# Kernel tuning notes

Hardware: AMD Instinct MI355X
Metric: run time of the kernel (lower is better)

Reference implementation:

```python
import jax, jax.numpy as jnp
import numpy as np

N_NODES = 100000
N_EDGES = 3200000
D = 256
REPEAT = 2
FACTOR = 0.5


def setup_inputs() -> dict:
    key = jax.random.key(0)
    k1, k2, k3, k4, k5, k6 = jax.random.split(key, 6)
    x = jax.random.normal(k1, (N_NODES, D), dtype=jnp.float32)
    vals = jax.random.uniform(k2, (N_EDGES,), dtype=jnp.float32)
    # Xavier-ish scale for linear weights
    W0 = jax.random.normal(k3, (D, D), dtype=jnp.float32) / np.sqrt(D)
    W1 = jax.random.normal(k4, (D, D), dtype=jnp.float32) / np.sqrt(D)
    rows = jax.random.randint(k5, (N_EDGES,), 0, N_NODES, dtype=jnp.int32)
    cols = jax.random.randint(k6, (N_EDGES,), 0, N_NODES, dtype=jnp.int32)
    return {"x": x, "vals": vals, "W0": W0, "W1": W1, "rows": rows, "cols": cols}


def reference(x, vals, W0, W1, rows, cols):
    # support is sparse [N, N] in COO: support[rows[e], cols[e]] = vals[e]
    def spmm(h):
        # gather source-node features, scale by edge weight, scatter-add to dst
        return jax.ops.segment_sum(vals[:, None] * h[cols], rows,
                                   num_segments=N_NODES)

    h = x
    for W, act in ((W0, jax.nn.relu), (W1, lambda v: v)):
        # _propagate: repeated SpMM with scalar factor
        for _ in range(REPEAT):
            h = spmm(h) * FACTOR
        # linear (no bias) + activation
        h = act(h @ W)
    return h
```

## Files before the change

kernel.cpp:

```cpp
#include <hip/hip_runtime.h>
#include <hip/hip_bf16.h>
#include <hip/hip_fp16.h>

#define N_D 256
#define NBLK 832
#define CPB 52
#define NCH 16
#define RPG_MAX 12512

typedef __attribute__((ext_vector_type(8))) short bf16x8;
typedef __attribute__((ext_vector_type(4))) float f32x4;

__device__ __forceinline__ unsigned short f2bf(float f) {
  union { float f; unsigned u; } c; c.f = f;
  unsigned u = c.u;
  return (unsigned short)((u + 0x7fffu + ((u >> 16) & 1u)) >> 16);
}
__device__ __forceinline__ float asf(unsigned u) {
  union { unsigned u; float f; } c; c.u = u;
  return c.f;
}
__device__ __forceinline__ int grp_of(int r, unsigned gmagic) {
  int g = (int)(((unsigned long long)(unsigned)r * gmagic) >> 37);
  return min(g, 7);
}

template <bool AF32>
__device__ __forceinline__ void gemm_core(
    const void* __restrict__ H, const unsigned short* __restrict__ WT,
    unsigned short* __restrict__ C, int M, int bid) {
  const int wave = threadIdx.x >> 6;
  const int lane = threadIdx.x & 63;
  const int m = lane & 15;
  const int p = lane >> 4;
  const int row0 = bid * 128 + wave * 32;

  f32x4 acc0[16], acc1[16];
#pragma unroll
  for (int i = 0; i < 16; ++i) {
    acc0[i] = (f32x4){0.f, 0.f, 0.f, 0.f};
    acc1[i] = (f32x4){0.f, 0.f, 0.f, 0.f};
  }

  const int r0 = row0 + m;
  const int r1 = row0 + 16 + m;
  const bool ok0 = r0 < M, ok1 = r1 < M;

  for (int k0 = 0; k0 < N_D; k0 += 32) {
    bf16x8 a0 = {0,0,0,0,0,0,0,0}, a1 = {0,0,0,0,0,0,0,0};
    if (AF32) {
      if (ok0) {
        const float* ap = (const float*)H + (size_t)r0 * N_D + k0 + p * 8;
        const float4 f0 = *reinterpret_cast<const float4*>(ap);
        const float4 f1 = *reinterpret_cast<const float4*>(ap + 4);
        a0[0]=f2bf(f0.x); a0[1]=f2bf(f0.y); a0[2]=f2bf(f0.z); a0[3]=f2bf(f0.w);
        a0[4]=f2bf(f1.x); a0[5]=f2bf(f1.y); a0[6]=f2bf(f1.z); a0[7]=f2bf(f1.w);
      }
      if (ok1) {
        const float* ap = (const float*)H + (size_t)r1 * N_D + k0 + p * 8;
        const float4 f0 = *reinterpret_cast<const float4*>(ap);
        const float4 f1 = *reinterpret_cast<const float4*>(ap + 4);
        a1[0]=f2bf(f0.x); a1[1]=f2bf(f0.y); a1[2]=f2bf(f0.z); a1[3]=f2bf(f0.w);
        a1[4]=f2bf(f1.x); a1[5]=f2bf(f1.y); a1[6]=f2bf(f1.z); a1[7]=f2bf(f1.w);
      }
    } else {
      if (ok0) a0 = *reinterpret_cast<const bf16x8*>(
          (const unsigned short*)H + (size_t)r0 * N_D + k0 + p * 8);
      if (ok1) a1 = *reinterpret_cast<const bf16x8*>(
          (const unsigned short*)H + (size_t)r1 * N_D + k0 + p * 8);
    }
#pragma unroll
    for (int nt = 0; nt < 16; ++nt) {
      const bf16x8 b = *reinterpret_cast<const bf16x8*>(
          WT + (size_t)(nt * 16 + m) * N_D + k0 + p * 8);
      acc0[nt] = __builtin_amdgcn_mfma_f32_16x16x32_bf16(a0, b, acc0[nt], 0, 0, 0);
      acc1[nt] = __builtin_amdgcn_mfma_f32_16x16x32_bf16(a1, b, acc1[nt], 0, 0, 0);
    }
  }

#pragma unroll
  for (int nt = 0; nt < 16; ++nt) {
    const int col = nt * 16 + m;
#pragma unroll
    for (int rr = 0; rr < 4; ++rr) {
      const int ra = row0 + p * 4 + rr;
      const int rb = ra + 16;
      if (ra < M) C[(size_t)ra * N_D + col] = f2bf(acc0[nt][rr]);
      if (rb < M) C[(size_t)rb * N_D + col] = f2bf(acc1[nt][rr]);
    }
  }
}

__global__ __launch_bounds__(256) void gemm3_bf16(
    const unsigned short* __restrict__ H, const unsigned short* __restrict__ WT,
    unsigned short* __restrict__ C, int M) {
  gemm_core<false>(H, WT, C, M, blockIdx.x);
}

__global__ __launch_bounds__(256) void p0_kernel(
    const int* __restrict__ rows, int* __restrict__ cntT,
    int n_edges, unsigned gmagic,
    const float* __restrict__ W0, const float* __restrict__ W1,
    unsigned short* __restrict__ WT0, unsigned short* __restrict__ WT1) {
  if (blockIdx.x >= NBLK) {
    const int b = blockIdx.x - NBLK;
    const int w = b >> 8;
    const int k = b & 255;
    const int n = threadIdx.x;
    const float* W = w ? W1 : W0;
    unsigned short* WT = w ? WT1 : WT0;
    WT[(size_t)n * N_D + k] = f2bf(W[(size_t)k * N_D + n]);
    return;
  }
  __shared__ int l8[8];
  if (threadIdx.x < 8) l8[threadIdx.x] = 0;
  __syncthreads();
  for (int e = blockIdx.x * 256 + threadIdx.x; e < n_edges; e += NBLK * 256) {
    atomicAdd(&l8[grp_of(rows[e], gmagic)], 1);
  }
  __syncthreads();
  if (threadIdx.x < 8) cntT[threadIdx.x * NBLK + blockIdx.x] = l8[threadIdx.x];
}

__global__ __launch_bounds__(256) void scan_one(
    const int* __restrict__ in, int* __restrict__ out, int n) {
  __shared__ int swsum[4];
  __shared__ int carry_sh;
  const int tid = threadIdx.x;
  const int lane = tid & 63;
  const int wid = tid >> 6;
  if (tid == 0) carry_sh = 0;
  __syncthreads();
  for (int base = 0; base < n; base += 1024) {
    const int i0 = base + tid * 4;
    int4 v = make_int4(0, 0, 0, 0);
    if (i0 + 3 < n) v = *reinterpret_cast<const int4*>(in + i0);
    else {
      if (i0     < n) v.x = in[i0];
      if (i0 + 1 < n) v.y = in[i0 + 1];
      if (i0 + 2 < n) v.z = in[i0 + 2];
    }
    const int s1 = v.x, s2 = s1 + v.y, s3 = s2 + v.z, s4 = s3 + v.w;
    int ws = s4;
#pragma unroll
    for (int off = 1; off < 64; off <<= 1) {
      int o = __shfl_up(ws, off, 64);
      if (lane >= off) ws += o;
    }
    if (lane == 63) swsum[wid] = ws;
    __syncthreads();
    if (wid == 0) {
      int t = (lane < 4) ? swsum[lane] : 0;
#pragma unroll
      for (int off = 1; off < 4; off <<= 1) {
        int o = __shfl_up(t, off, 64);
        if (lane >= off) t += o;
      }
      if (lane < 4) swsum[lane] = t;
    }
    __syncthreads();
    const int carry = carry_sh;
    const int tbase = carry + (wid ? swsum[wid - 1] : 0) + ws - s4;
    if (i0     < n) out[i0]     = tbase;
    if (i0 + 1 < n) out[i0 + 1] = tbase + s1;
    if (i0 + 2 < n) out[i0 + 2] = tbase + s2;
    if (i0 + 3 < n) out[i0 + 3] = tbase + s3;
    __syncthreads();
    if (tid == 0) carry_sh = carry + swsum[3];
    __syncthreads();
  }
  if (tid == 0) out[n] = carry_sh;
}

__global__ __launch_bounds__(256) void fatpg_kernel(
    const int* __restrict__ rows, const int* __restrict__ cols,
    const float* __restrict__ vals, const int* __restrict__ pofsT,
    int2* __restrict__ part, int n_edges, unsigned gmagic,
    const float* __restrict__ x, const unsigned short* __restrict__ WT0,
    unsigned short* __restrict__ hB, int M) {
  if (blockIdx.x >= NBLK) {
    gemm_core<true>(x, WT0, hB, M, blockIdx.x - NBLK);
    return;
  }
  __shared__ int lofs[8];
  if (threadIdx.x < 8) lofs[threadIdx.x] = pofsT[threadIdx.x * NBLK + blockIdx.x];
  __syncthreads();
  for (int e = blockIdx.x * 256 + threadIdx.x; e < n_edges; e += NBLK * 256) {
    const int r = rows[e];
    const int g = grp_of(r, gmagic);
    const int slot = atomicAdd(&lofs[g], 1);
    const unsigned short hb = __half_as_ushort(__float2half_rn(vals[e] * 0.5f));
    int2 rv;
    rv.x = r;
    rv.y = (int)(((unsigned)cols[e] << 15) | ((unsigned)hb >> 1));
    part[slot] = rv;
  }
}

__global__ __launch_bounds__(256) void hist_kernel(
    const int2* __restrict__ part, const int* __restrict__ pofsT,
    int* __restrict__ cntc, int M, int rpg) {
  const int g = blockIdx.x & 7;
  const int b = blockIdx.x >> 3;
  const int r0 = g * rpg;
  const int nr = min(rpg, M - r0);
  __shared__ int lh[RPG_MAX];
  for (int r = threadIdx.x; r < nr; r += 256) lh[r] = 0;
  __syncthreads();
  const int s0 = pofsT[g * NBLK + b * CPB];
  const int s1 = pofsT[g * NBLK + (b + 1) * CPB];
  for (int i = s0 + threadIdx.x; i < s1; i += 256) {
    atomicAdd(&lh[part[i].x - r0], 1);
  }
  __syncthreads();
  int* dst = cntc + (size_t)(g * NCH + b) * rpg;
  for (int r = threadIdx.x; r < nr; r += 256) dst[r] = lh[r];
}

__global__ __launch_bounds__(256) void sumcnt2_kernel(
    int* __restrict__ cntc, int* __restrict__ cnts,
    int* __restrict__ bsum, int M, int rpg) {
  __shared__ int wred[4];
  const int i = blockIdx.x * 256 + threadIdx.x;
  int s = 0;
  if (i < M) {
    const int g = i / rpg;
    const int rr = i - g * rpg;
    int* base = cntc + (size_t)g * NCH * rpg + rr;
#pragma unroll
    for (int b = 0; b < NCH; ++b) {
      const int c = base[(size_t)b * rpg];
      base[(size_t)b * rpg] = s;
      s += c;
    }
    cnts[i] = s;
  }
  int t = s;
#pragma unroll
  for (int off = 32; off; off >>= 1) t += __shfl_down(t, off, 64);
  if ((threadIdx.x & 63) == 0) wred[threadIdx.x >> 6] = t;
  __syncthreads();
  if (threadIdx.x == 0) bsum[blockIdx.x] = wred[0] + wred[1] + wred[2] + wred[3];
}

__global__ __launch_bounds__(256) void apply_kernel(
    const int* __restrict__ cnts, const int* __restrict__ bofs,
    int* __restrict__ row_ptr, int M) {
  __shared__ int wsum[4];
  const int tid = threadIdx.x;
  const int lane = tid & 63;
  const int wid = tid >> 6;
  const int i = blockIdx.x * 256 + tid;
  const int v = (i < M) ? cnts[i] : 0;
  int s = v;
#pragma unroll
  for (int off = 1; off < 64; off <<= 1) {
    int o = __shfl_up(s, off, 64);
    if (lane >= off) s += o;
  }
  if (lane == 63) wsum[wid] = s;
  __syncthreads();
  int add = 0;
  for (int k = 0; k < wid; ++k) add += wsum[k];
  const int excl = bofs[blockIdx.x] + add + s - v;
  if (i < M) row_ptr[i] = excl;
  if (i == M) row_ptr[M] = bofs[gridDim.x];
}

__global__ __launch_bounds__(256) void scatter3_kernel(
    const int2* __restrict__ part, const int* __restrict__ pofsT,
    const int* __restrict__ row_ptr, const int* __restrict__ cntc,
    unsigned* __restrict__ colpack, int M, int rpg) {
  const int g = blockIdx.x & 7;
  const int b = blockIdx.x >> 3;
  const int r0 = g * rpg;
  const int nr = min(rpg, M - r0);
  __shared__ int lc[RPG_MAX];
  const int* pfx = cntc + (size_t)(g * NCH + b) * rpg;
  for (int r = threadIdx.x; r < nr; r += 256)
    lc[r] = row_ptr[r0 + r] + pfx[r];
  __syncthreads();
  const int s0 = pofsT[g * NBLK + b * CPB];
  const int s1 = pofsT[g * NBLK + (b + 1) * CPB];
  for (int i = s0 + threadIdx.x; i < s1; i += 256) {
    const int2 rv = part[i];
    const int pos = atomicAdd(&lc[rv.x - r0], 1);
    colpack[pos] = (unsigned)rv.y;
  }
}

template <bool RELU, bool F32OUT>
__global__ __launch_bounds__(256) void spmm_slice(
    const unsigned short* __restrict__ hin, const int* __restrict__ row_ptr,
    const unsigned* __restrict__ colpack, void* __restrict__ hout,
    int n_nodes) {
  const int slice = blockIdx.x & 3;
  const int lane = threadIdx.x & 63;
  const int half = lane >> 5;
  const int sub  = lane & 31;
  const int wgid = ((blockIdx.x >> 2) * 256 + threadIdx.x) >> 6;
  const int node = wgid * 2 + half;
  const bool ok = node < n_nodes;
  int start = 0, end = 0;
  if (ok) { start = row_ptr[node]; end = row_ptr[node + 1]; }

  const unsigned* __restrict__ hinw = reinterpret_cast<const unsigned*>(hin);
  const int fofs = slice * 32 + sub;
  const int sbase = half << 5;

  float acc0 = 0.f, acc1 = 0.f;

  for (int base = start; base < end; base += 32) {
    const int cnt = min(32, end - base);
    unsigned u = 0;
    if (base + sub < end) u = __builtin_nontemporal_load(&colpack[base + sub]);
    for (int t = 0; t < cnt; t += 8) {
      unsigned hv[8];
      float v[8];
#pragma unroll
      for (int j = 0; j < 8; ++j) {
        const unsigned ue = (unsigned)__shfl((int)u, sbase + t + j, 64);
        const int c = (int)(ue >> 15);
        v[j] = __half2float(__ushort_as_half((unsigned short)(ue << 1)));
        hv[j] = hinw[(size_t)c * 128 + fofs];
      }
#pragma unroll
      for (int j = 0; j < 8; ++j) {
        acc0 += v[j] * asf(hv[j] << 16);
        acc1 += v[j] * asf(hv[j] & 0xffff0000u);
      }
    }
  }
  if (ok) {
    if (RELU) { acc0 = fmaxf(acc0, 0.f); acc1 = fmaxf(acc1, 0.f); }
    if (F32OUT) {
      reinterpret_cast<float2*>(hout)[(size_t)node * 128 + fofs] =
          make_float2(acc0, acc1);
    } else {
      reinterpret_cast<unsigned*>(hout)[(size_t)node * 128 + fofs] =
          (unsigned)f2bf(acc0) | ((unsigned)f2bf(acc1) << 16);
    }
  }
}

extern "C" void kernel_launch(void* const* d_in, const int* in_sizes, int n_in,
                              void* d_out, int out_size, void* d_ws, size_t ws_size,
                              hipStream_t stream) {
  const float* x    = (const float*)d_in[0];
  const float* vals = (const float*)d_in[1];
  const float* W0   = (const float*)d_in[2];
  const float* W1   = (const float*)d_in[3];
  const int*   rows = (const int*)d_in[4];
  const int*   cols = (const int*)d_in[5];

  const int n_edges = in_sizes[1];
  const int M = in_sizes[0] / N_D;
  const size_t n_feat = (size_t)M * N_D;

  char* ws = (char*)d_ws;
  unsigned short* hA      = (unsigned short*)(ws);
  unsigned*       colpack = (unsigned*)(ws + 51200000);
  int*            row_ptr = (int*)(ws + 64000000);
  int*            cnts    = (int*)(ws + 64400128);
  int*            bsum    = (int*)(ws + 64800256);
  int*            bofs    = (int*)(ws + 64802816);
  int*            cntT    = (int*)(ws + 64805376);
  int*            pofsT   = (int*)(ws + 64832000);
  unsigned short* wt0     = (unsigned short*)(ws + 64858880);
  unsigned short* wt1     = (unsigned short*)(ws + 64989952);
  unsigned short* hB   = (unsigned short*)d_out;
  unsigned short* hC   = (unsigned short*)d_out + n_feat;
  int2*           part = (int2*)((char*)d_out + 51200000);
  int*            cntc = (int*)((char*)d_out + 76800000);

  const int Mb = (M + 255) / 256;
  const int sblocks = 4 * ((M + 7) / 8);
  const int gblocks = (M + 127) / 128;
  const int rpg = (M + 7) / 8;
  const unsigned gmagic = (unsigned)(((1ULL << 37) + rpg - 1) / (unsigned long long)rpg);

  p0_kernel<<<NBLK + 512, 256, 0, stream>>>(rows, cntT, n_edges, gmagic,
                                            W0, W1, wt0, wt1);
  scan_one<<<1, 256, 0, stream>>>(cntT, pofsT, 8 * NBLK);
  fatpg_kernel<<<NBLK + gblocks, 256, 0, stream>>>(rows, cols, vals, pofsT, part,
                                                   n_edges, gmagic, x, wt0, hB, M);
  hist_kernel<<<8 * NCH, 256, 0, stream>>>(part, pofsT, cntc, M, rpg);
  sumcnt2_kernel<<<Mb, 256, 0, stream>>>(cntc, cnts, bsum, M, rpg);
  scan_one<<<1, 256, 0, stream>>>(bsum, bofs, Mb);
  apply_kernel<<<Mb, 256, 0, stream>>>(cnts, bofs, row_ptr, M);
  scatter3_kernel<<<8 * NCH, 256, 0, stream>>>(part, pofsT, row_ptr, cntc,
                                               colpack, M, rpg);

  spmm_slice<false, false><<<sblocks, 256, 0, stream>>>(hB, row_ptr, colpack, hA, M);
  spmm_slice<true,  false><<<sblocks, 256, 0, stream>>>(hA, row_ptr, colpack, hB, M);

  gemm3_bf16<<<gblocks, 256, 0, stream>>>(hB, wt1, hC, M);
  spmm_slice<false, false><<<sblocks, 256, 0, stream>>>(hC, row_ptr, colpack, hA, M);
  spmm_slice<false, true ><<<sblocks, 256, 0, stream>>>(hA, row_ptr, colpack, d_out, M);
}
```

Measured before the change: 1.077 ms.

## Partition edges in contiguous chunks with LDS staging for coalesced writes

Counting and partitioning now give each block a contiguous range of 4096 edges instead of a grid-strided one. Rows, cols and vals are read with vector loads. The partition kernel bins each 512-edge sub-chunk into per-group shared-memory buffers and then writes each group's run contiguously, replacing scattered 8-byte global writes. The first GEMM is split out of the fused partition launch into its own kernel, so the two no longer overlap within one launch but each kernel is simpler.

```diff
diff --git a/kernel.cpp b/kernel.cpp
--- a/kernel.cpp
+++ b/kernel.cpp
@@ -7,6 +7,8 @@
 #define CPB 52
 #define NCH 16
 #define RPG_MAX 12512
+#define EPB 4096
+#define PR 512
 
 typedef __attribute__((ext_vector_type(8))) short bf16x8;
 typedef __attribute__((ext_vector_type(4))) float f32x4;
@@ -23,6 +25,10 @@
 __device__ __forceinline__ int grp_of(int r, unsigned gmagic) {
   int g = (int)(((unsigned long long)(unsigned)r * gmagic) >> 37);
   return min(g, 7);
+}
+__device__ __forceinline__ unsigned packcv(int c, float vl) {
+  const unsigned short hb = __half_as_ushort(__float2half_rn(vl * 0.5f));
+  return ((unsigned)c << 15) | ((unsigned)hb >> 1);
 }
 
 template <bool AF32>
@@ -91,6 +97,11 @@
   }
 }
 
+__global__ __launch_bounds__(256) void gemm3_f32(
+    const float* __restrict__ H, const unsigned short* __restrict__ WT,
+    unsigned short* __restrict__ C, int M) {
+  gemm_core<true>(H, WT, C, M, blockIdx.x);
+}
 __global__ __launch_bounds__(256) void gemm3_bf16(
     const unsigned short* __restrict__ H, const unsigned short* __restrict__ WT,
     unsigned short* __restrict__ C, int M) {
@@ -115,8 +126,19 @@
   __shared__ int l8[8];
   if (threadIdx.x < 8) l8[threadIdx.x] = 0;
   __syncthreads();
-  for (int e = blockIdx.x * 256 + threadIdx.x; e < n_edges; e += NBLK * 256) {
-    atomicAdd(&l8[grp_of(rows[e], gmagic)], 1);
+  const int e0 = blockIdx.x * EPB;
+  const int e1 = min(n_edges, e0 + EPB);
+  for (int e = e0 + threadIdx.x * 4; e < e1; e += 1024) {
+    if (e + 3 < e1) {
+      const int4 v = *reinterpret_cast<const int4*>(rows + e);
+      atomicAdd(&l8[grp_of(v.x, gmagic)], 1);
+      atomicAdd(&l8[grp_of(v.y, gmagic)], 1);
+      atomicAdd(&l8[grp_of(v.z, gmagic)], 1);
+      atomicAdd(&l8[grp_of(v.w, gmagic)], 1);
+    } else {
+      for (int k = 0; k < 4 && e + k < e1; ++k)
+        atomicAdd(&l8[grp_of(rows[e + k], gmagic)], 1);
+    }
   }
   __syncthreads();
   if (threadIdx.x < 8) cntT[threadIdx.x * NBLK + blockIdx.x] = l8[threadIdx.x];
@@ -172,28 +194,51 @@
   if (tid == 0) out[n] = carry_sh;
 }
 
-__global__ __launch_bounds__(256) void fatpg_kernel(
+__global__ __launch_bounds__(256) void partition_kernel(
     const int* __restrict__ rows, const int* __restrict__ cols,
     const float* __restrict__ vals, const int* __restrict__ pofsT,
-    int2* __restrict__ part, int n_edges, unsigned gmagic,
-    const float* __restrict__ x, const unsigned short* __restrict__ WT0,
-    unsigned short* __restrict__ hB, int M) {
-  if (blockIdx.x >= NBLK) {
-    gemm_core<true>(x, WT0, hB, M, blockIdx.x - NBLK);
-    return;
-  }
+    int2* __restrict__ part, int n_edges, unsigned gmagic) {
   __shared__ int lofs[8];
-  if (threadIdx.x < 8) lofs[threadIdx.x] = pofsT[threadIdx.x * NBLK + blockIdx.x];
-  __syncthreads();
-  for (int e = blockIdx.x * 256 + threadIdx.x; e < n_edges; e += NBLK * 256) {
-    const int r = rows[e];
-    const int g = grp_of(r, gmagic);
-    const int slot = atomicAdd(&lofs[g], 1);
-    const unsigned short hb = __half_as_ushort(__float2half_rn(vals[e] * 0.5f));
-    int2 rv;
-    rv.x = r;
-    rv.y = (int)(((unsigned)cols[e] << 15) | ((unsigned)hb >> 1));
-    part[slot] = rv;
+  __shared__ int lcnt[8];
+  __shared__ int2 lbuf[8][PR];
+  const int tid = threadIdx.x;
+  const int bid = blockIdx.x;
+  if (tid < 8) lofs[tid] = pofsT[tid * NBLK + bid];
+  const int e0 = bid * EPB;
+  const int e1 = min(n_edges, e0 + EPB);
+  for (int base = e0; base < e1; base += PR) {
+    if (tid < 8) lcnt[tid] = 0;
+    __syncthreads();
+    const int e = base + tid * 2;
+    if (e < e1) {
+      int2 rr, cc; float2 vv;
+      const bool two = (e + 1 < e1);
+      if (two) {
+        rr = *reinterpret_cast<const int2*>(rows + e);
+        cc = *reinterpret_cast<const int2*>(cols + e);
+        vv = *reinterpret_cast<const float2*>(vals + e);
+      } else {
+        rr.x = rows[e]; cc.x = cols[e]; vv.x = vals[e];
+      }
+      {
+        const int g = grp_of(rr.x, gmagic);
+        const int slot = atomicAdd(&lcnt[g], 1);
+        lbuf[g][slot] = make_int2(rr.x, (int)packcv(cc.x, vv.x));
+      }
+      if (two) {
+        const int g = grp_of(rr.y, gmagic);
+        const int slot = atomicAdd(&lcnt[g], 1);
+        lbuf[g][slot] = make_int2(rr.y, (int)packcv(cc.y, vv.y));
+      }
+    }
+    __syncthreads();
+    for (int g = 0; g < 8; ++g) {
+      const int c = lcnt[g];
+      const int o = lofs[g];
+      for (int i = tid; i < c; i += 256) part[o + i] = lbuf[g][i];
+    }
+    __syncthreads();
+    if (tid < 8) lofs[tid] += lcnt[tid];
   }
 }
 
@@ -382,8 +427,9 @@
   p0_kernel<<<NBLK + 512, 256, 0, stream>>>(rows, cntT, n_edges, gmagic,
                                             W0, W1, wt0, wt1);
   scan_one<<<1, 256, 0, stream>>>(cntT, pofsT, 8 * NBLK);
-  fatpg_kernel<<<NBLK + gblocks, 256, 0, stream>>>(rows, cols, vals, pofsT, part,
-                                                   n_edges, gmagic, x, wt0, hB, M);
+  gemm3_f32<<<gblocks, 256, 0, stream>>>(x, wt0, hB, M);
+  partition_kernel<<<NBLK, 256, 0, stream>>>(rows, cols, vals, pofsT, part,
+                                             n_edges, gmagic);
   hist_kernel<<<8 * NCH, 256, 0, stream>>>(part, pofsT, cntc, M, rpg);
   sumcnt2_kernel<<<Mb, 256, 0, stream>>>(cntc, cnts, bsum, M, rpg);
   scan_one<<<1, 256, 0, stream>>>(bsum, bofs, Mb);
```

New measurement: 1.059 ms, median of 2. About the same (-1.6%).
